# Optimization experiments

Hardware: AMD Instinct MI355X
Metric: run time of the kernel (lower is better)

Reference implementation:

```python
import jax, jax.numpy as jnp
import numpy as np

B, S, D = 2, 2048, 2048
H, KVH = 16, 4
HD = D // H            # 128
N_REP = H // KVH       # 4


def apply_rope(x, cos, sin):
    # x: (b, s, h, hd); cos/sin: (1, s, 1, hd//2)
    b, s, h, hd = x.shape
    xr = x.reshape(b, s, h, hd // 2, 2)
    p1, p2 = xr[..., 0], xr[..., 1]
    # Original concatenates rotated halves (does NOT re-interleave).
    return jnp.concatenate([p1 * cos - p2 * sin, p2 * cos + p1 * sin], axis=-1)


def setup_inputs() -> dict:
    key = jax.random.key(0)
    ks = jax.random.split(key, 8)
    hidden_states = jax.random.normal(ks[0], (B, S, D), dtype=jnp.float32)
    # additive causal mask (0 on/below diagonal, -1e9 above)
    mask = jnp.where(jnp.tril(jnp.ones((S, S), dtype=bool)), 0.0, -1e9).astype(jnp.float32)
    attention_mask = mask[None, None, :, :]
    cos = jax.random.normal(ks[1], (1, S, 1, HD // 2), dtype=jnp.float32)
    sin = jax.random.normal(ks[2], (1, S, 1, HD // 2), dtype=jnp.float32)
    sc = 1.0 / np.sqrt(D)
    Wq = jax.random.normal(ks[3], (D, H * HD), dtype=jnp.float32) * sc
    Wk = jax.random.normal(ks[4], (D, KVH * HD), dtype=jnp.float32) * sc
    Wv = jax.random.normal(ks[5], (D, KVH * HD), dtype=jnp.float32) * sc
    Wo = jax.random.normal(ks[6], (H * HD, D), dtype=jnp.float32) * sc
    return {"hidden_states": hidden_states, "attention_mask": attention_mask,
            "cos": cos, "sin": sin, "Wq": Wq, "Wk": Wk, "Wv": Wv, "Wo": Wo}


def reference(hidden_states, attention_mask, cos, sin, Wq, Wk, Wv, Wo):
    b, s, _ = hidden_states.shape
    q = (hidden_states @ Wq).reshape(b, s, H, HD)
    k = (hidden_states @ Wk).reshape(b, s, KVH, HD)
    v = (hidden_states @ Wv).reshape(b, s, KVH, HD)
    q = apply_rope(q, cos, sin)
    k = apply_rope(k, cos, sin)
    # GQA: repeat kv heads contiguously (matches expand+reshape)
    k = jnp.repeat(k, N_REP, axis=2)
    v = jnp.repeat(v, N_REP, axis=2)
    # (b, h, s, hd)
    q = q.transpose(0, 2, 1, 3)
    k = k.transpose(0, 2, 1, 3)
    v = v.transpose(0, 2, 1, 3)
    scores = jnp.einsum('bhqd,bhkd->bhqk', q, k) / np.sqrt(HD).astype(np.float32)
    scores = scores + attention_mask
    attn = jax.nn.softmax(scores.astype(jnp.float32), axis=-1)
    out = jnp.einsum('bhqk,bhkd->bhqd', attn, v)
    out = out.transpose(0, 2, 1, 3).reshape(b, s, H * HD)
    return out @ Wo
```

## Files before the change

kernel.cpp:

```cpp
#include <hip/hip_runtime.h>
#include <cstddef>
#include <cstdint>

#define S_LEN 2048
#define DMODEL 2048
#define NH 16
#define NKV 4
#define HD 128
#define BATCH 2
#define MROWS (BATCH * S_LEN)
#define KVD (NKV * HD)
#define QKVSTR 3072
#define NQT (S_LEN / 64)

typedef __attribute__((ext_vector_type(8))) short bf16x8;
typedef __attribute__((ext_vector_type(4))) float floatx4;
typedef __attribute__((ext_vector_type(8))) _Float16 half8;
typedef __attribute__((ext_vector_type(4))) _Float16 half4;
typedef __attribute__((ext_vector_type(2))) _Float16 half2v;

#define QSCALE 0.1275310255f

__device__ inline short f2bf(float f) {
  union { float f; unsigned u; } v; v.f = f;
  unsigned r = v.u + 0x7FFFu + ((v.u >> 16) & 1u);
  return (short)(r >> 16);
}

__device__ inline half2v pack2h(float lo, float hi) {
  union { decltype(__builtin_amdgcn_cvt_pkrtz(0.f, 0.f)) raw; half2v h; } u;
  u.raw = __builtin_amdgcn_cvt_pkrtz(lo, hi);
  return u.h;
}

__device__ __forceinline__ void glds16(const void* g, void* l) {
  __builtin_amdgcn_global_load_lds(
      reinterpret_cast<const int __attribute__((address_space(1)))*>(
          reinterpret_cast<uintptr_t>(g)),
      reinterpret_cast<int __attribute__((address_space(3)))*>(
          reinterpret_cast<uintptr_t>(l)),
      16, 0, 0);
}

__global__ __launch_bounds__(256) void cast_bf16(
    const float* __restrict__ x, short* __restrict__ y)
{
  const size_t i = ((size_t)blockIdx.x * 256 + threadIdx.x) * 8;
  const float4 a = *(const float4*)(x + i);
  const float4 b = *(const float4*)(x + i + 4);
  bf16x8 o;
  o[0] = f2bf(a.x); o[1] = f2bf(a.y); o[2] = f2bf(a.z); o[3] = f2bf(a.w);
  o[4] = f2bf(b.x); o[5] = f2bf(b.y); o[6] = f2bf(b.z); o[7] = f2bf(b.w);
  *(bf16x8*)(y + i) = o;
}

__global__ __launch_bounds__(256) void tcast(
    const float* __restrict__ W, short* __restrict__ Wt, int N)
{
  __shared__ float Ts[64][65];
  const int n0 = blockIdx.x * 64, k0 = blockIdx.y * 64;
  const int tid = threadIdx.x;
#pragma unroll
  for (int it = 0; it < 4; ++it) {
    const int r = it * 16 + (tid >> 4);
    *(float4*)&Ts[r][(tid & 15) * 4] =
        *(const float4*)&W[(size_t)(k0 + r) * N + n0 + (tid & 15) * 4];
  }
  __syncthreads();
  const int n = tid >> 2, kg = (tid & 3) * 16;
  bf16x8 o0, o1;
#pragma unroll
  for (int e = 0; e < 8; ++e) o0[e] = f2bf(Ts[kg + e][n]);
#pragma unroll
  for (int e = 0; e < 8; ++e) o1[e] = f2bf(Ts[kg + 8 + e][n]);
  short* dst = Wt + (size_t)(n0 + n) * DMODEL + k0 + kg;
  *(bf16x8*)dst = o0;
  *(bf16x8*)(dst + 8) = o1;
}

template <bool OUTF16>
__global__ __launch_bounds__(256) void gemm_glds(
    const short* __restrict__ A, const short* __restrict__ Bt,
    void* __restrict__ Cv, int M, int N, int K)
{
  __shared__ short As[128 * 64];
  __shared__ short Bs[128 * 64];

  const int tid = threadIdx.x;
  const int wave = tid >> 6, lane = tid & 63;
  const int l16 = lane & 15, quad = lane >> 4;
  const int wm = (wave & 1) * 64, wn = (wave >> 1) * 64;
  const int m0 = blockIdx.y * 128, n0 = blockIdx.x * 128;

  const short* Ab = A + (size_t)(m0 + wave * 32 + (lane >> 3)) * K + ((lane & 7) << 3);
  const short* Bb = Bt + (size_t)(n0 + wave * 32 + (lane >> 3)) * K + ((lane & 7) << 3);
  short* Asw = As + wave * 32 * 64;
  short* Bsw = Bs + wave * 32 * 64;

  floatx4 acc[4][4];
#pragma unroll
  for (int i = 0; i < 4; ++i)
#pragma unroll
    for (int j = 0; j < 4; ++j)
#pragma unroll
      for (int r = 0; r < 4; ++r) acc[i][j][r] = 0.f;

  for (int k0 = 0; k0 < K; k0 += 64) {
    __syncthreads();
#pragma unroll
    for (int u = 0; u < 4; ++u) {
      glds16(Ab + (size_t)(u * 8) * K + k0, Asw + u * 8 * 64);
      glds16(Bb + (size_t)(u * 8) * K + k0, Bsw + u * 8 * 64);
    }
    __syncthreads();
#pragma unroll
    for (int c = 0; c < 2; ++c) {
      bf16x8 af[4], bf[4];
#pragma unroll
      for (int i = 0; i < 4; ++i)
        af[i] = *(const bf16x8*)&As[(wm + i * 16 + l16) * 64 + c * 32 + quad * 8];
#pragma unroll
      for (int j = 0; j < 4; ++j)
        bf[j] = *(const bf16x8*)&Bs[(wn + j * 16 + l16) * 64 + c * 32 + quad * 8];
#pragma unroll
      for (int i = 0; i < 4; ++i)
#pragma unroll
        for (int j = 0; j < 4; ++j)
          acc[i][j] = __builtin_amdgcn_mfma_f32_16x16x32_bf16(af[i], bf[j], acc[i][j], 0, 0, 0);
    }
  }

#pragma unroll
  for (int i = 0; i < 4; ++i)
#pragma unroll
    for (int r = 0; r < 4; ++r) {
      const int row = m0 + wm + i * 16 + (quad << 2) + r;
      if (OUTF16) {
        _Float16* cr = (_Float16*)Cv + (size_t)row * N + n0 + wn + l16;
#pragma unroll
        for (int j = 0; j < 4; ++j) cr[j * 16] = (_Float16)acc[i][j][r];
      } else {
        float* cr = (float*)Cv + (size_t)row * N + n0 + wn + l16;
#pragma unroll
        for (int j = 0; j < 4; ++j) cr[j * 16] = acc[i][j][r];
      }
    }
}

__global__ __launch_bounds__(256) void rope_k(
    _Float16* __restrict__ kh, const float* __restrict__ cosp,
    const float* __restrict__ sinp)
{
  const int row = blockIdx.x * 4 + (threadIdx.x >> 6);
  const int sl = row & (S_LEN - 1);
  const int t = threadIdx.x & 63;
  const int h = t >> 4, g = t & 15;
  _Float16* base = kh + (size_t)row * QKVSTR + h * HD;
  const half8 x = *(const half8*)(base + 8 * g);
  const float4 c4 = *(const float4*)&cosp[sl * 64 + 4 * g];
  const float4 s4 = *(const float4*)&sinp[sl * 64 + 4 * g];
  const float p1[4] = {(float)x[0], (float)x[2], (float)x[4], (float)x[6]};
  const float p2[4] = {(float)x[1], (float)x[3], (float)x[5], (float)x[7]};
  const float cc[4] = {c4.x, c4.y, c4.z, c4.w};
  const float ss[4] = {s4.x, s4.y, s4.z, s4.w};
  __syncthreads();
  half4 o1, o2;
#pragma unroll
  for (int u = 0; u < 4; ++u) {
    o1[u] = (_Float16)(p1[u] * cc[u] - p2[u] * ss[u]);
    o2[u] = (_Float16)(p2[u] * cc[u] + p1[u] * ss[u]);
  }
  *(half4*)(base + 4 * g) = o1;
  *(half4*)(base + 64 + 4 * g) = o2;
}

__global__ __launch_bounds__(256) void vtprep(
    const _Float16* __restrict__ v, _Float16* __restrict__ Vt)
{
  __shared__ _Float16 Ts[64][72];
  const int s0 = blockIdx.x * 64, c0 = blockIdx.y * 64;
  const int tid = threadIdx.x;
#pragma unroll
  for (int it = 0; it < 4; ++it) {
    const int r = it * 16 + (tid >> 4);
    *(half4*)&Ts[r][(tid & 15) * 4] =
        *(const half4*)&v[(size_t)(s0 + r) * QKVSTR + c0 + (tid & 15) * 4];
  }
  __syncthreads();
  const int dr = tid >> 2, sg = tid & 3;
  const int d = c0 + dr;
  const int kvh = d >> 7, dd = d & 127;
  const int bb = s0 >> 11, sl = s0 & (S_LEN - 1);
  half8 t0, t1;
#pragma unroll
  for (int kk = 0; kk < 8; ++kk) t0[kk] = Ts[sg * 16 + kk][dr];
#pragma unroll
  for (int kk = 0; kk < 8; ++kk) t1[kk] = Ts[sg * 16 + 8 + kk][dr];
  _Float16* dst = Vt + ((size_t)(bb * NKV + kvh) * HD + dd) * S_LEN + sl + sg * 16;
  *(half8*)dst = t0;
  *(half8*)(dst + 8) = t1;
}

__global__ __launch_bounds__(256, 2) void attn_mfma(
    const _Float16* __restrict__ Qh, const _Float16* __restrict__ Kr,
    const _Float16* __restrict__ Vt, const float* __restrict__ cosp,
    const float* __restrict__ sinp, short* __restrict__ aout)
{
  __shared__ _Float16 Ks[2][64][136];
  __shared__ _Float16 Vs[2][128][72];
  __shared__ _Float16 Ps[4][16][72];

  const int tid = threadIdx.x;
  const int wave = tid >> 6, lane = tid & 63;
  const int l16 = lane & 15, quad = lane >> 4;
  const int pair = blockIdx.x;
  const int h = blockIdx.y, b = blockIdx.z;
  const int kvh = h >> 2;

  const int skr = tid >> 2;
  const int skc = (tid & 3) * 32;
  const _Float16* kgp = Kr + (size_t)(b * S_LEN + skr) * QKVSTR + kvh * HD + skc;
  const int svr = tid >> 1;
  const int svc = (tid & 1) * 32;
  const _Float16* vgp = Vt + ((size_t)(b * NKV + kvh) * HD + svr) * S_LEN + svc;

  for (int pass = 0; pass < 2; ++pass) {
    const int qt = pass ? (NQT - 1 - pair) : pair;
    const int q0 = qt * 64 + wave * 16;
    const int srow = q0 + l16;

    half8 qf[4];
    {
      const _Float16* qraw = Qh + (size_t)(b * S_LEN + srow) * QKVSTR + h * HD;
#pragma unroll
      for (int cc = 0; cc < 2; ++cc) {
        const half8 r0 = *(const half8*)(qraw + cc * 64 + quad * 16);
        const half8 r1 = *(const half8*)(qraw + cc * 64 + quad * 16 + 8);
        const float4 c0 = *(const float4*)&cosp[srow % S_LEN * 64 + cc * 32 + quad * 8];
        const float4 c1 = *(const float4*)&cosp[srow % S_LEN * 64 + cc * 32 + quad * 8 + 4];
        const float4 s0 = *(const float4*)&sinp[srow % S_LEN * 64 + cc * 32 + quad * 8];
        const float4 s1 = *(const float4*)&sinp[srow % S_LEN * 64 + cc * 32 + quad * 8 + 4];
        const float cA[8] = {c0.x, c0.y, c0.z, c0.w, c1.x, c1.y, c1.z, c1.w};
        const float sA[8] = {s0.x, s0.y, s0.z, s0.w, s1.x, s1.y, s1.z, s1.w};
#pragma unroll
        for (int j = 0; j < 8; ++j) {
          const float p1 = (float)((j < 4) ? r0[2 * j] : r1[2 * (j - 4)]);
          const float p2 = (float)((j < 4) ? r0[2 * j + 1] : r1[2 * (j - 4) + 1]);
          qf[cc][j]     = (_Float16)((p1 * cA[j] - p2 * sA[j]) * QSCALE);
          qf[cc + 2][j] = (_Float16)((p2 * cA[j] + p1 * sA[j]) * QSCALE);
        }
      }
    }

    floatx4 o[8];
#pragma unroll
    for (int d = 0; d < 8; ++d) o[d] = (floatx4){0.f, 0.f, 0.f, 0.f};
    float m_run[4] = {-3e38f, -3e38f, -3e38f, -3e38f};
    float l_run[4] = {0.f, 0.f, 0.f, 0.f};

    __syncthreads();
    {
      _Float16* dst = &Ks[0][skr][skc];
#pragma unroll
      for (int u = 0; u < 4; ++u)
        *(half8*)(dst + u * 8) = *(const half8*)(kgp + u * 8);
      _Float16* dv = &Vs[0][svr][svc];
#pragma unroll
      for (int u = 0; u < 4; ++u)
        *(half8*)(dv + u * 8) = *(const half8*)(vgp + u * 8);
    }
    __syncthreads();

    int cur = 0;
    for (int kt = 0; kt <= qt; ++kt) {
      const int k0 = kt * 64;
      const bool pre = (kt < qt);

      half8 kreg[4], vreg[4];
      if (pre) {
        const _Float16* g = kgp + (size_t)(kt + 1) * 64 * QKVSTR;
#pragma unroll
        for (int u = 0; u < 4; ++u) kreg[u] = *(const half8*)(g + u * 8);
        const _Float16* gv = vgp + (kt + 1) * 64;
#pragma unroll
        for (int u = 0; u < 4; ++u) vreg[u] = *(const half8*)(gv + u * 8);
      }

      const _Float16 (*Kc)[136] = Ks[cur];
      const _Float16 (*Vc)[72]  = Vs[cur];

      floatx4 s[4];
      __builtin_amdgcn_s_setprio(1);
#pragma unroll
      for (int i = 0; i < 4; ++i) {
        s[i] = (floatx4){0.f, 0.f, 0.f, 0.f};
#pragma unroll
        for (int c = 0; c < 4; ++c) {
          const half8 kf = *(const half8*)&Kc[i * 16 + l16][quad * 8 + c * 32];
          s[i] = __builtin_amdgcn_mfma_f32_16x16x32_f16(qf[c], kf, s[i], 0, 0, 0);
        }
      }
      __builtin_amdgcn_s_setprio(0);

      if (kt == qt) {
#pragma unroll
        for (int i = 0; i < 4; ++i) {
          const int kpos = k0 + i * 16 + l16;
#pragma unroll
          for (int r = 0; r < 4; ++r)
            if (kpos > q0 + quad * 4 + r) s[i][r] = -3.0e38f;
        }
      }

      float p[4][4];
#pragma unroll
      for (int r = 0; r < 4; ++r) {
        float rm = fmaxf(fmaxf(s[0][r], s[1][r]), fmaxf(s[2][r], s[3][r]));
        rm = fmaxf(rm, __shfl_xor(rm, 1));
        rm = fmaxf(rm, __shfl_xor(rm, 2));
        rm = fmaxf(rm, __shfl_xor(rm, 4));
        rm = fmaxf(rm, __shfl_xor(rm, 8));
        if (rm > m_run[r]) {
          const float alpha = exp2f(m_run[r] - rm);
          m_run[r] = rm;
          l_run[r] *= alpha;
#pragma unroll
          for (int d = 0; d < 8; ++d) o[d][r] *= alpha;
        }
        float rs = 0.f;
#pragma unroll
        for (int i = 0; i < 4; ++i) { p[i][r] = exp2f(s[i][r] - m_run[r]); rs += p[i][r]; }
        rs += __shfl_xor(rs, 1);
        rs += __shfl_xor(rs, 2);
        rs += __shfl_xor(rs, 4);
        rs += __shfl_xor(rs, 8);
        l_run[r] += rs;
      }

      const int odd = l16 & 1;
      const int cbase = l16 & 14;
#pragma unroll
      for (int i = 0; i < 4; ++i) {
#pragma unroll
        for (int rr = 0; rr < 2; ++rr) {
          const float send = odd ? p[i][rr] : p[i][2 + rr];
          const float recv = __shfl_xor(send, 1);
          const float lo = odd ? recv : p[i][rr];
          const float hi = odd ? p[i][2 + rr] : recv;
          *(half2v*)&Ps[wave][quad * 4 + 2 * odd + rr][i * 16 + cbase] = pack2h(lo, hi);
        }
      }
      const half8 pf0 = *(const half8*)&Ps[wave][l16][quad * 8];
      const half8 pf1 = *(const half8*)&Ps[wave][l16][32 + quad * 8];

      __builtin_amdgcn_s_setprio(1);
#pragma unroll
      for (int d = 0; d < 8; ++d) {
        const half8 vf0 = *(const half8*)&Vc[d * 16 + l16][quad * 8];
        const half8 vf1 = *(const half8*)&Vc[d * 16 + l16][32 + quad * 8];
        o[d] = __builtin_amdgcn_mfma_f32_16x16x32_f16(pf0, vf0, o[d], 0, 0, 0);
        o[d] = __builtin_amdgcn_mfma_f32_16x16x32_f16(pf1, vf1, o[d], 0, 0, 0);
      }
      __builtin_amdgcn_s_setprio(0);

      if (pre) {
        _Float16* dst = &Ks[cur ^ 1][skr][skc];
#pragma unroll
        for (int u = 0; u < 4; ++u) *(half8*)(dst + u * 8) = kreg[u];
        _Float16* dv = &Vs[cur ^ 1][svr][svc];
#pragma unroll
        for (int u = 0; u < 4; ++u) *(half8*)(dv + u * 8) = vreg[u];
      }
      __syncthreads();
      cur ^= 1;
    }

    float inv[4];
#pragma unroll
    for (int r = 0; r < 4; ++r) inv[r] = 1.0f / l_run[r];
#pragma unroll
    for (int d = 0; d < 8; ++d)
#pragma unroll
      for (int r = 0; r < 4; ++r)
        aout[(size_t)(b * S_LEN + q0 + quad * 4 + r) * DMODEL + h * HD + d * 16 + l16] =
            f2bf(o[d][r] * inv[r]);
  }
}

extern "C" void kernel_launch(void* const* d_in, const int* in_sizes, int n_in,
                              void* d_out, int out_size, void* d_ws, size_t ws_size,
                              hipStream_t stream) {
  const float* hs   = (const float*)d_in[0];
  const float* cosp = (const float*)d_in[2];
  const float* sinp = (const float*)d_in[3];
  const float* Wq   = (const float*)d_in[4];
  const float* Wk   = (const float*)d_in[5];
  const float* Wv   = (const float*)d_in[6];
  const float* Wo   = (const float*)d_in[7];
  float* out = (float*)d_out;

  char* w = (char*)d_ws;
  short*    hsb = (short*)w;
  short*    Wt  = (short*)(w + 16777216);
  _Float16* qkv = (_Float16*)(w + 29360128);
  _Float16* Vt  = (_Float16*)(w + 54525952);
  short*    ao  = hsb;

  _Float16* qh = qkv;
  _Float16* kh = qkv + 2048;
  _Float16* vh = qkv + 2560;

  dim3 blk(256);
  cast_bf16<<<MROWS * DMODEL / (8 * 256), blk, 0, stream>>>(hs, hsb);
  tcast<<<dim3(DMODEL / 64, DMODEL / 64), blk, 0, stream>>>(Wq, Wt, DMODEL);
  tcast<<<dim3(KVD / 64, DMODEL / 64), blk, 0, stream>>>(Wk, Wt + (size_t)2048 * DMODEL, KVD);
  tcast<<<dim3(KVD / 64, DMODEL / 64), blk, 0, stream>>>(Wv, Wt + (size_t)2560 * DMODEL, KVD);
  gemm_glds<true><<<dim3(QKVSTR / 128, MROWS / 128), blk, 0, stream>>>(hsb, Wt, qkv, MROWS, QKVSTR, DMODEL);
  rope_k<<<MROWS / 4, blk, 0, stream>>>(kh, cosp, sinp);
  vtprep<<<dim3(MROWS / 64, KVD / 64), blk, 0, stream>>>(vh, Vt);
  attn_mfma<<<dim3(NQT / 2, NH, BATCH), blk, 0, stream>>>(qh, kh, Vt, cosp, sinp, ao);
  tcast<<<dim3(DMODEL / 64, DMODEL / 64), blk, 0, stream>>>(Wo, Wt, DMODEL);
  gemm_glds<false><<<dim3(DMODEL / 128, MROWS / 128), blk, 0, stream>>>(ao, Wt, out, MROWS, DMODEL, DMODEL);
}
```

Measured before the change: 396.1 us.

## Enlarge attention query tile to 128 rows, two 16-row slices per wave

Each attention block now handles 128 query rows instead of 64, with every wave computing two 16-row sub-tiles. Each K/V fragment loaded from shared memory feeds twice as many MFMAs, which halves K/V global and LDS traffic per query row. The cost is more registers (launch bounds drop to one block per SM) and half as many blocks (256), which could leave many of the 256 CUs underfilled and lowers occupancy.

```diff
diff --git a/kernel.cpp b/kernel.cpp
--- a/kernel.cpp
+++ b/kernel.cpp
@@ -11,7 +11,7 @@
 #define MROWS (BATCH * S_LEN)
 #define KVD (NKV * HD)
 #define QKVSTR 3072
-#define NQT (S_LEN / 64)
+#define NQT128 (S_LEN / 128)
 
 typedef __attribute__((ext_vector_type(8))) short bf16x8;
 typedef __attribute__((ext_vector_type(4))) float floatx4;
@@ -201,14 +201,14 @@
   *(half8*)(dst + 8) = t1;
 }
 
-__global__ __launch_bounds__(256, 2) void attn_mfma(
+__global__ __launch_bounds__(256, 1) void attn_mfma(
     const _Float16* __restrict__ Qh, const _Float16* __restrict__ Kr,
     const _Float16* __restrict__ Vt, const float* __restrict__ cosp,
     const float* __restrict__ sinp, short* __restrict__ aout)
 {
   __shared__ _Float16 Ks[2][64][136];
   __shared__ _Float16 Vs[2][128][72];
-  __shared__ _Float16 Ps[4][16][72];
+  __shared__ _Float16 Ps[4][32][72];
 
   const int tid = threadIdx.x;
   const int wave = tid >> 6, lane = tid & 63;
@@ -225,38 +225,45 @@
   const _Float16* vgp = Vt + ((size_t)(b * NKV + kvh) * HD + svr) * S_LEN + svc;
 
   for (int pass = 0; pass < 2; ++pass) {
-    const int qt = pass ? (NQT - 1 - pair) : pair;
-    const int q0 = qt * 64 + wave * 16;
-    const int srow = q0 + l16;
-
-    half8 qf[4];
-    {
+    const int qt = pass ? (NQT128 - 1 - pair) : pair;
+    const int qbase = qt * 128 + wave * 32;
+
+    half8 qf[2][4];
+#pragma unroll
+    for (int r16 = 0; r16 < 2; ++r16) {
+      const int srow = qbase + r16 * 16 + l16;
       const _Float16* qraw = Qh + (size_t)(b * S_LEN + srow) * QKVSTR + h * HD;
+      const int co = (srow & (S_LEN - 1)) * 64;
 #pragma unroll
       for (int cc = 0; cc < 2; ++cc) {
         const half8 r0 = *(const half8*)(qraw + cc * 64 + quad * 16);
         const half8 r1 = *(const half8*)(qraw + cc * 64 + quad * 16 + 8);
-        const float4 c0 = *(const float4*)&cosp[srow % S_LEN * 64 + cc * 32 + quad * 8];
-        const float4 c1 = *(const float4*)&cosp[srow % S_LEN * 64 + cc * 32 + quad * 8 + 4];
-        const float4 s0 = *(const float4*)&sinp[srow % S_LEN * 64 + cc * 32 + quad * 8];
-        const float4 s1 = *(const float4*)&sinp[srow % S_LEN * 64 + cc * 32 + quad * 8 + 4];
+        const float4 c0 = *(const float4*)&cosp[co + cc * 32 + quad * 8];
+        const float4 c1 = *(const float4*)&cosp[co + cc * 32 + quad * 8 + 4];
+        const float4 s0 = *(const float4*)&sinp[co + cc * 32 + quad * 8];
+        const float4 s1 = *(const float4*)&sinp[co + cc * 32 + quad * 8 + 4];
         const float cA[8] = {c0.x, c0.y, c0.z, c0.w, c1.x, c1.y, c1.z, c1.w};
         const float sA[8] = {s0.x, s0.y, s0.z, s0.w, s1.x, s1.y, s1.z, s1.w};
 #pragma unroll
         for (int j = 0; j < 8; ++j) {
           const float p1 = (float)((j < 4) ? r0[2 * j] : r1[2 * (j - 4)]);
           const float p2 = (float)((j < 4) ? r0[2 * j + 1] : r1[2 * (j - 4) + 1]);
-          qf[cc][j]     = (_Float16)((p1 * cA[j] - p2 * sA[j]) * QSCALE);
-          qf[cc + 2][j] = (_Float16)((p2 * cA[j] + p1 * sA[j]) * QSCALE);
+          qf[r16][cc][j]     = (_Float16)((p1 * cA[j] - p2 * sA[j]) * QSCALE);
+          qf[r16][cc + 2][j] = (_Float16)((p2 * cA[j] + p1 * sA[j]) * QSCALE);
         }
       }
     }
 
-    floatx4 o[8];
-#pragma unroll
-    for (int d = 0; d < 8; ++d) o[d] = (floatx4){0.f, 0.f, 0.f, 0.f};
-    float m_run[4] = {-3e38f, -3e38f, -3e38f, -3e38f};
-    float l_run[4] = {0.f, 0.f, 0.f, 0.f};
+    floatx4 o[2][8];
+#pragma unroll
+    for (int r16 = 0; r16 < 2; ++r16)
+#pragma unroll
+      for (int d = 0; d < 8; ++d) o[r16][d] = (floatx4){0.f, 0.f, 0.f, 0.f};
+    float m_run[2][4], l_run[2][4];
+#pragma unroll
+    for (int r16 = 0; r16 < 2; ++r16)
+#pragma unroll
+      for (int r = 0; r < 4; ++r) { m_run[r16][r] = -3e38f; l_run[r16][r] = 0.f; }
 
     __syncthreads();
     {
@@ -271,10 +278,11 @@
     }
     __syncthreads();
 
+    const int ktmax = 2 * qt + 1;
     int cur = 0;
-    for (int kt = 0; kt <= qt; ++kt) {
+    for (int kt = 0; kt <= ktmax; ++kt) {
       const int k0 = kt * 64;
-      const bool pre = (kt < qt);
+      const bool pre = (kt < ktmax);
 
       half8 kreg[4], vreg[4];
       if (pre) {
@@ -286,80 +294,97 @@
         for (int u = 0; u < 4; ++u) vreg[u] = *(const half8*)(gv + u * 8);
       }
 
-      const _Float16 (*Kc)[136] = Ks[cur];
-      const _Float16 (*Vc)[72]  = Vs[cur];
-
-      floatx4 s[4];
+      floatx4 s[2][4];
+#pragma unroll
+      for (int r16 = 0; r16 < 2; ++r16)
+#pragma unroll
+        for (int i = 0; i < 4; ++i) s[r16][i] = (floatx4){0.f, 0.f, 0.f, 0.f};
       __builtin_amdgcn_s_setprio(1);
 #pragma unroll
-      for (int i = 0; i < 4; ++i) {
-        s[i] = (floatx4){0.f, 0.f, 0.f, 0.f};
+      for (int i = 0; i < 4; ++i)
 #pragma unroll
         for (int c = 0; c < 4; ++c) {
-          const half8 kf = *(const half8*)&Kc[i * 16 + l16][quad * 8 + c * 32];
-          s[i] = __builtin_amdgcn_mfma_f32_16x16x32_f16(qf[c], kf, s[i], 0, 0, 0);
+          const half8 kf = *(const half8*)&Ks[cur][i * 16 + l16][quad * 8 + c * 32];
+          s[0][i] = __builtin_amdgcn_mfma_f32_16x16x32_f16(qf[0][c], kf, s[0][i], 0, 0, 0);
+          s[1][i] = __builtin_amdgcn_mfma_f32_16x16x32_f16(qf[1][c], kf, s[1][i], 0, 0, 0);
         }
-      }
       __builtin_amdgcn_s_setprio(0);
 
-      if (kt == qt) {
-#pragma unroll
-        for (int i = 0; i < 4; ++i) {
-          const int kpos = k0 + i * 16 + l16;
-#pragma unroll
-          for (int r = 0; r < 4; ++r)
-            if (kpos > q0 + quad * 4 + r) s[i][r] = -3.0e38f;
+      if (kt >= 2 * qt) {
+#pragma unroll
+        for (int r16 = 0; r16 < 2; ++r16)
+#pragma unroll
+          for (int i = 0; i < 4; ++i) {
+            const int kpos = k0 + i * 16 + l16;
+#pragma unroll
+            for (int r = 0; r < 4; ++r)
+              if (kpos > qbase + r16 * 16 + quad * 4 + r) s[r16][i][r] = -3.0e38f;
+          }
+      }
+
+      float p[2][4][4];
+#pragma unroll
+      for (int r16 = 0; r16 < 2; ++r16)
+#pragma unroll
+        for (int r = 0; r < 4; ++r) {
+          float rm = fmaxf(fmaxf(s[r16][0][r], s[r16][1][r]),
+                           fmaxf(s[r16][2][r], s[r16][3][r]));
+          rm = fmaxf(rm, __shfl_xor(rm, 1));
+          rm = fmaxf(rm, __shfl_xor(rm, 2));
+          rm = fmaxf(rm, __shfl_xor(rm, 4));
+          rm = fmaxf(rm, __shfl_xor(rm, 8));
+          if (rm > m_run[r16][r]) {
+            const float alpha = exp2f(m_run[r16][r] - rm);
+            m_run[r16][r] = rm;
+            l_run[r16][r] *= alpha;
+#pragma unroll
+            for (int d = 0; d < 8; ++d) o[r16][d][r] *= alpha;
+          }
+          float rs = 0.f;
+#pragma unroll
+          for (int i = 0; i < 4; ++i) {
+            p[r16][i][r] = exp2f(s[r16][i][r] - m_run[r16][r]);
+            rs += p[r16][i][r];
+          }
+          rs += __shfl_xor(rs, 1);
+          rs += __shfl_xor(rs, 2);
+          rs += __shfl_xor(rs, 4);
+          rs += __shfl_xor(rs, 8);
+          l_run[r16][r] += rs;
         }
-      }
-
-      float p[4][4];
-#pragma unroll
-      for (int r = 0; r < 4; ++r) {
-        float rm = fmaxf(fmaxf(s[0][r], s[1][r]), fmaxf(s[2][r], s[3][r]));
-        rm = fmaxf(rm, __shfl_xor(rm, 1));
-        rm = fmaxf(rm, __shfl_xor(rm, 2));
-        rm = fmaxf(rm, __shfl_xor(rm, 4));
-        rm = fmaxf(rm, __shfl_xor(rm, 8));
-        if (rm > m_run[r]) {
-          const float alpha = exp2f(m_run[r] - rm);
-          m_run[r] = rm;
-          l_run[r] *= alpha;
-#pragma unroll
-          for (int d = 0; d < 8; ++d) o[d][r] *= alpha;
-        }
-        float rs = 0.f;
-#pragma unroll
-        for (int i = 0; i < 4; ++i) { p[i][r] = exp2f(s[i][r] - m_run[r]); rs += p[i][r]; }
-        rs += __shfl_xor(rs, 1);
-        rs += __shfl_xor(rs, 2);
-        rs += __shfl_xor(rs, 4);
-        rs += __shfl_xor(rs, 8);
-        l_run[r] += rs;
-      }
 
       const int odd = l16 & 1;
       const int cbase = l16 & 14;
 #pragma unroll
-      for (int i = 0; i < 4; ++i) {
-#pragma unroll
-        for (int rr = 0; rr < 2; ++rr) {
-          const float send = odd ? p[i][rr] : p[i][2 + rr];
-          const float recv = __shfl_xor(send, 1);
-          const float lo = odd ? recv : p[i][rr];
-          const float hi = odd ? p[i][2 + rr] : recv;
-          *(half2v*)&Ps[wave][quad * 4 + 2 * odd + rr][i * 16 + cbase] = pack2h(lo, hi);
+      for (int r16 = 0; r16 < 2; ++r16)
+#pragma unroll
+        for (int i = 0; i < 4; ++i) {
+#pragma unroll
+          for (int rr = 0; rr < 2; ++rr) {
+            const float send = odd ? p[r16][i][rr] : p[r16][i][2 + rr];
+            const float recv = __shfl_xor(send, 1);
+            const float lo = odd ? recv : p[r16][i][rr];
+            const float hi = odd ? p[r16][i][2 + rr] : recv;
+            *(half2v*)&Ps[wave][r16 * 16 + quad * 4 + 2 * odd + rr][i * 16 + cbase] =
+                pack2h(lo, hi);
+          }
         }
-      }
-      const half8 pf0 = *(const half8*)&Ps[wave][l16][quad * 8];
-      const half8 pf1 = *(const half8*)&Ps[wave][l16][32 + quad * 8];
+      half8 pf[2][2];
+#pragma unroll
+      for (int r16 = 0; r16 < 2; ++r16) {
+        pf[r16][0] = *(const half8*)&Ps[wave][r16 * 16 + l16][quad * 8];
+        pf[r16][1] = *(const half8*)&Ps[wave][r16 * 16 + l16][32 + quad * 8];
+      }
 
       __builtin_amdgcn_s_setprio(1);
 #pragma unroll
       for (int d = 0; d < 8; ++d) {
-        const half8 vf0 = *(const half8*)&Vc[d * 16 + l16][quad * 8];
-        const half8 vf1 = *(const half8*)&Vc[d * 16 + l16][32 + quad * 8];
-        o[d] = __builtin_amdgcn_mfma_f32_16x16x32_f16(pf0, vf0, o[d], 0, 0, 0);
-        o[d] = __builtin_amdgcn_mfma_f32_16x16x32_f16(pf1, vf1, o[d], 0, 0, 0);
+        const half8 vf0 = *(const half8*)&Vs[cur][d * 16 + l16][quad * 8];
+        const half8 vf1 = *(const half8*)&Vs[cur][d * 16 + l16][32 + quad * 8];
+        o[0][d] = __builtin_amdgcn_mfma_f32_16x16x32_f16(pf[0][0], vf0, o[0][d], 0, 0, 0);
+        o[0][d] = __builtin_amdgcn_mfma_f32_16x16x32_f16(pf[0][1], vf1, o[0][d], 0, 0, 0);
+        o[1][d] = __builtin_amdgcn_mfma_f32_16x16x32_f16(pf[1][0], vf0, o[1][d], 0, 0, 0);
+        o[1][d] = __builtin_amdgcn_mfma_f32_16x16x32_f16(pf[1][1], vf1, o[1][d], 0, 0, 0);
       }
       __builtin_amdgcn_s_setprio(0);
 
@@ -375,15 +400,18 @@
       cur ^= 1;
     }
 
-    float inv[4];
-#pragma unroll
-    for (int r = 0; r < 4; ++r) inv[r] = 1.0f / l_run[r];
-#pragma unroll
-    for (int d = 0; d < 8; ++d)
-#pragma unroll
-      for (int r = 0; r < 4; ++r)
-        aout[(size_t)(b * S_LEN + q0 + quad * 4 + r) * DMODEL + h * HD + d * 16 + l16] =
-            f2bf(o[d][r] * inv[r]);
+#pragma unroll
+    for (int r16 = 0; r16 < 2; ++r16) {
+      float inv[4];
+#pragma unroll
+      for (int r = 0; r < 4; ++r) inv[r] = 1.0f / l_run[r16][r];
+#pragma unroll
+      for (int d = 0; d < 8; ++d)
+#pragma unroll
+        for (int r = 0; r < 4; ++r)
+          aout[(size_t)(b * S_LEN + qbase + r16 * 16 + quad * 4 + r) * DMODEL +
+               h * HD + d * 16 + l16] = f2bf(o[r16][d][r] * inv[r]);
+    }
   }
 }
 
@@ -418,7 +446,7 @@
   gemm_glds<true><<<dim3(QKVSTR / 128, MROWS / 128), blk, 0, stream>>>(hsb, Wt, qkv, MROWS, QKVSTR, DMODEL);
   rope_k<<<MROWS / 4, blk, 0, stream>>>(kh, cosp, sinp);
   vtprep<<<dim3(MROWS / 64, KVD / 64), blk, 0, stream>>>(vh, Vt);
-  attn_mfma<<<dim3(NQT / 2, NH, BATCH), blk, 0, stream>>>(qh, kh, Vt, cosp, sinp, ao);
+  attn_mfma<<<dim3(NQT128 / 2, NH, BATCH), blk, 0, stream>>>(qh, kh, Vt, cosp, sinp, ao);
   tcast<<<dim3(DMODEL / 64, DMODEL / 64), blk, 0, stream>>>(Wo, Wt, DMODEL);
   gemm_glds<false><<<dim3(DMODEL / 128, MROWS / 128), blk, 0, stream>>>(ao, Wt, out, MROWS, DMODEL, DMODEL);
 }
```

Result: slower. 435.4 us (+9.9%).
